# Kernel optimization log

Measured on AMD Instinct MI355X. Metric: run time of the kernel, lower is better.

Reference implementation:

```python
import jax, jax.numpy as jnp
import numpy as np

B, S, DIM = 4, 2048, 512
HEADS, DHEAD = 8, 64
INNER = HEADS * DHEAD


def setup_inputs() -> dict:
    key = jax.random.key(0)
    k1, k2, k3, k4 = jax.random.split(key, 4)
    x = jax.random.normal(k1, (B, S, DIM), dtype=jnp.float32)
    W_qkv = jax.random.normal(k2, (DIM, 3 * INNER), dtype=jnp.float32) * (DIM ** -0.5)
    W_out = jax.random.normal(k3, (INNER, DIM), dtype=jnp.float32) * (INNER ** -0.5)
    b_out = jnp.zeros((DIM,), dtype=jnp.float32)
    # learnable log-temperature, initialized to log(dim_head**-0.5)
    log_temp = jnp.asarray(np.log(DHEAD ** -0.5), dtype=jnp.float32)
    return {"x": x, "W_qkv": W_qkv, "log_temp": log_temp, "W_out": W_out, "b_out": b_out}


def reference(x, W_qkv, log_temp, W_out, b_out):
    b, s, _ = x.shape
    qkv = x @ W_qkv  # [b, s, 3*inner]
    q, k, v = jnp.split(qkv, 3, axis=-1)
    # [b, s, inner] -> [b, h, s, d]
    reshape = lambda t: t.reshape(b, s, HEADS, DHEAD).transpose(0, 2, 1, 3)
    q, k, v = reshape(q), reshape(k), reshape(v)
    dots = jnp.einsum("bhid,bhjd->bhij", q, k) * jnp.exp(log_temp)
    mask_value = -jnp.finfo(dots.dtype).max
    eye = jnp.eye(s, dtype=bool)
    dots = jnp.where(eye, mask_value, dots)
    attn = jax.nn.softmax(dots, axis=-1)
    out = jnp.einsum("bhij,bhjd->bhid", attn, v)
    out = out.transpose(0, 2, 1, 3).reshape(b, s, INNER)
    return out @ W_out + b_out
```

## Files before the change

### kernel.cpp

```cpp
#include <hip/hip_runtime.h>
#include <hip/hip_bf16.h>

#define BB 4
#define SS 2048
#define DIMM 512
#define HH 8
#define DD 64
#define NQKV 1536

typedef float  floatx4 __attribute__((ext_vector_type(4)));
typedef short  bf16x8  __attribute__((ext_vector_type(8)));
typedef short  bf16x4  __attribute__((ext_vector_type(4)));

#define MFMA16(A, B, C) __builtin_amdgcn_mfma_f32_16x16x32_bf16(A, B, C, 0, 0, 0)

__device__ __forceinline__ floatx4 MFMA16K16(bf16x4 a, bf16x4 b, floatx4 c) {
#if __has_builtin(__builtin_amdgcn_mfma_f32_16x16x16bf16_1k)
    return __builtin_amdgcn_mfma_f32_16x16x16bf16_1k(a, b, c, 0, 0, 0);
#else
    floatx4 d;
    asm volatile("v_mfma_f32_16x16x16_bf16 %0, %1, %2, %3"
                 : "=v"(d) : "v"(a), "v"(b), "v"(c));
    return d;
#endif
}

__device__ __forceinline__ unsigned short f2bf(float f) {
    unsigned int u = __float_as_uint(f);
    u += 0x7FFFu + ((u >> 16) & 1u);
    return (unsigned short)(u >> 16);
}

__device__ __forceinline__ unsigned int f2bf_pk(float lo, float hi) {
    float2 f; f.x = lo; f.y = hi;
    __hip_bfloat162 h = __float22bfloat162_rn(f);
    return *reinterpret_cast<unsigned int*>(&h);
}

__device__ __forceinline__ float fast_exp2(float x) {
#if __has_builtin(__builtin_amdgcn_exp2f)
    return __builtin_amdgcn_exp2f(x);
#else
    return __exp2f(x);
#endif
}

__device__ __forceinline__ void gl_lds16(const void* g, void* l) {
    __builtin_amdgcn_global_load_lds(
        (__attribute__((address_space(1))) void*)g,
        (__attribute__((address_space(3))) void*)l,
        16, 0, 0);
}

__global__ __launch_bounds__(256) void k_prep(
    const float* __restrict__ x, const float* __restrict__ W_qkv,
    const float* __restrict__ W_out,
    unsigned short* __restrict__ xb, unsigned short* __restrict__ Wq_t,
    unsigned short* __restrict__ Wo_t) {
    __shared__ float t[32][33];
    int bid = blockIdx.x, tid = threadIdx.x;
    if (bid < 4096) {
        int i = (bid * 256 + tid) * 4;
        float4 v = *(const float4*)(x + i);
        ushort4 o;
        o.x = f2bf(v.x); o.y = f2bf(v.y); o.z = f2bf(v.z); o.w = f2bf(v.w);
        *(ushort4*)(xb + i) = o;
        return;
    }
    const float* in; unsigned short* out; int R = 512, C, bx, by;
    if (bid < 4864) { in = W_qkv; out = Wq_t; C = 1536; int blk = bid - 4096; bx = blk % 48; by = blk / 48; }
    else            { in = W_out; out = Wo_t; C = 512;  int blk = bid - 4864; bx = blk % 16; by = blk / 16; }
    int tx = tid & 31, ty = tid >> 5;
    int c0 = bx * 32, r0 = by * 32;
    for (int i = 0; i < 4; i++) {
        int r = r0 + ty + i * 8;
        t[ty + i * 8][tx] = in[(size_t)r * C + c0 + tx];
    }
    __syncthreads();
    for (int i = 0; i < 4; i++) {
        int cc = c0 + ty + i * 8;
        out[(size_t)cc * R + r0 + tx] = f2bf(t[tx][ty + i * 8]);
    }
}

__global__ __launch_bounds__(256) void k_gemm_qkv(
    const unsigned short* __restrict__ A,
    const unsigned short* __restrict__ Bt,
    const float* __restrict__ log_temp,
    unsigned short* __restrict__ Qb,
    unsigned short* __restrict__ Kb,
    unsigned short* __restrict__ Vt) {
    __shared__ unsigned short smem[2][128 * 64];
    unsigned short* As = smem[0];
    unsigned short* Bs = smem[1];
    const int K = 512;
    int m0 = blockIdx.x * 128, n0 = blockIdx.y * 128;
    int tid = threadIdx.x;
    int w = tid >> 6, lane = tid & 63;
    int c = lane & 15, q4 = lane >> 4;
    int wm = w >> 1, wn = w & 1;
    float qscale = __expf(log_temp[0]) * 1.44269504f;

    floatx4 acc[4][4] = {};

    for (int k0 = 0; k0 < K; k0 += 64) {
        __syncthreads();
        for (int i = 0; i < 4; i++) {
            int cidx = w * 256 + i * 64 + lane;
            int row = cidx >> 3, cc = cidx & 7;
            int gcc = cc ^ (row & 7);
            gl_lds16(A + (size_t)(m0 + row) * K + k0 + gcc * 8,
                     As + (size_t)(w * 256 + i * 64) * 8);
            gl_lds16(Bt + (size_t)(n0 + row) * K + k0 + gcc * 8,
                     Bs + (size_t)(w * 256 + i * 64) * 8);
        }
        __syncthreads();
        bf16x8 aF[2][4], bF[2][4];
        for (int kh = 0; kh < 2; kh++)
            for (int mt = 0; mt < 4; mt++) {
                int row = wm * 64 + mt * 16 + c;
                aF[kh][mt] = *(const bf16x8*)&As[row * 64 + (((kh * 4 + q4) ^ (row & 7)) * 8)];
            }
        for (int kh = 0; kh < 2; kh++)
            for (int nt = 0; nt < 4; nt++) {
                int row = wn * 64 + nt * 16 + c;
                bF[kh][nt] = *(const bf16x8*)&Bs[row * 64 + (((kh * 4 + q4) ^ (row & 7)) * 8)];
            }
        for (int kh = 0; kh < 2; kh++)
            for (int mt = 0; mt < 4; mt++)
                for (int nt = 0; nt < 4; nt++)
                    acc[mt][nt] = MFMA16(aF[kh][mt], bF[kh][nt], acc[mt][nt]);
    }

    if (n0 < 1024) {
        for (int nt = 0; nt < 4; nt++) {
            int n = n0 + wn * 64 + nt * 16 + c;
            int t = n >> 9, inner = n & 511;
            int h = inner >> 6, d = inner & 63;
            for (int mt = 0; mt < 4; mt++) {
                for (int r = 0; r < 4; r++) {
                    int m = m0 + wm * 64 + mt * 16 + q4 * 4 + r;
                    int b = m >> 11, s = m & 2047;
                    int bh = b * 8 + h;
                    float v = acc[mt][nt][r];
                    if (t == 0)  Qb[((size_t)bh * SS + s) * 64 + d] = f2bf(v * qscale);
                    else         Kb[((size_t)bh * SS + s) * 64 + d] = f2bf(v);
                }
            }
        }
    } else {
        unsigned short* T = &smem[0][0];
        int b = m0 >> 11, s_base = m0 & 2047;
        for (int half = 0; half < 2; half++) {
            __syncthreads();
            if (wn == half) {
                for (int nt = 0; nt < 4; nt++)
                    for (int mt = 0; mt < 4; mt++)
                        for (int r = 0; r < 4; r++)
                            T[(nt * 16 + c) * 136 + wm * 64 + mt * 16 + q4 * 4 + r] =
                                f2bf(acc[mt][nt][r]);
            }
            __syncthreads();
            for (int rr = 0; rr < 4; rr++) {
                int nl = w * 16 + rr * 4 + q4;
                int ml = c * 8;
                bf16x8 v = *(const bf16x8*)&T[nl * 136 + ml];
                int n = n0 + half * 64 + nl;
                int h = (n >> 6) - 16, d = n & 63;
                int bh = b * 8 + h;
                *(bf16x8*)(Vt + ((size_t)bh * 64 + d) * SS + s_base + ml) = v;
            }
        }
    }
}

__global__ __launch_bounds__(256, 2) void k_attn(
    const unsigned short* __restrict__ Qb,
    const unsigned short* __restrict__ Kb,
    const unsigned short* __restrict__ Vt,
    unsigned short* __restrict__ AO) {
    __shared__ unsigned short Ks[3][64 * 64];
    __shared__ unsigned short Vs[3][64 * 64];
    int q0 = blockIdx.x * 128;
    int h = blockIdx.y, b = blockIdx.z;
    int bh = b * 8 + h;
    int tid = threadIdx.x, w = tid >> 6, lane = tid & 63;
    int c = lane & 15, q4 = lane >> 4;

    const unsigned short* Kbase = Kb + (size_t)bh * SS * 64;
    const unsigned short* Vbase = Vt + (size_t)bh * 64 * SS;

    bf16x8 qf[2][2];
    for (int mi = 0; mi < 2; mi++) {
        const unsigned short* qp = Qb + ((size_t)bh * SS + q0 + w * 32 + mi * 16 + c) * 64;
        qf[mi][0] = *(const bf16x8*)(qp + q4 * 8);
        qf[mi][1] = *(const bf16x8*)(qp + 32 + q4 * 8);
    }

    const unsigned short* ksrc[2];
    const unsigned short* vsrc[2];
    int ldst[2];
    for (int i = 0; i < 2; i++) {
        int cidx = i * 256 + tid;
        int grow = cidx >> 3, gcc = (cidx & 7) ^ (grow & 7);
        ksrc[i] = Kbase + (size_t)grow * 64 + gcc * 8;
        vsrc[i] = Vbase + (size_t)grow * SS + gcc * 8;
        ldst[i] = (i * 256 + w * 64) * 8;
    }

    for (int i = 0; i < 2; i++) {
        gl_lds16(ksrc[i], &Ks[0][ldst[i]]);
        gl_lds16(vsrc[i], &Vs[0][ldst[i]]);
    }
    for (int i = 0; i < 2; i++) {
        gl_lds16(ksrc[i] + (size_t)64 * 64, &Ks[1][ldst[i]]);
        gl_lds16(vsrc[i] + 64, &Vs[1][ldst[i]]);
    }

    int koff0 = (q4 ^ (c & 7)) * 8;
    int koff1 = ((4 + q4) ^ (c & 7)) * 8;
    int vsub = (q4 & 1) * 4;
    int vchunk0 = (q4 >> 1);

    int mask_j0 = (q0 + w * 32) & ~63;
    int mglob0 = q0 + w * 32 + c;
    int mglob1 = mglob0 + 16;
    floatx4 oacc[2][4] = {};
    float psum0 = 0.f, psum1 = 0.f;

    int buf = 0;
    for (int j0 = 0; j0 < SS; j0 += 64) {
        if (j0 + 64 < SS) {
            asm volatile("s_waitcnt vmcnt(4)" ::: "memory");
        } else {
            asm volatile("s_waitcnt vmcnt(0)" ::: "memory");
        }
        asm volatile("s_barrier" ::: "memory");

        int jn = j0 + 128;
        if (jn < SS) {
            int bufn = buf + 2; if (bufn >= 3) bufn -= 3;
            for (int i = 0; i < 2; i++) {
                gl_lds16(ksrc[i] + (size_t)jn * 64, &Ks[bufn][ldst[i]]);
                gl_lds16(vsrc[i] + jn, &Vs[bufn][ldst[i]]);
            }
        }

        bool diag = (j0 == mask_j0);
        const unsigned short* KsB = Ks[buf];
        const unsigned short* VsB = Vs[buf];

#pragma unroll
        for (int jt = 0; jt < 4; jt++) {
            int rowoff = (jt * 16 + c) * 64;
            bf16x8 kf0 = *(const bf16x8*)&KsB[rowoff + koff0];
            bf16x8 kf1 = *(const bf16x8*)&KsB[rowoff + koff1];
            floatx4 sa0 = {}, sa1 = {};
            sa0 = MFMA16(kf0, qf[0][0], sa0);
            sa0 = MFMA16(kf1, qf[0][1], sa0);
            sa1 = MFMA16(kf0, qf[1][0], sa1);
            sa1 = MFMA16(kf1, qf[1][1], sa1);

            if (diag) {
#pragma unroll
                for (int r = 0; r < 4; r++) {
                    int jg = j0 + jt * 16 + q4 * 4 + r;
                    if (jg == mglob0) sa0[r] = -1e30f;
                    if (jg == mglob1) sa1[r] = -1e30f;
                }
            }

            float e0 = fast_exp2(sa0[0]), e1 = fast_exp2(sa0[1]);
            float e2 = fast_exp2(sa0[2]), e3 = fast_exp2(sa0[3]);
            psum0 += (e0 + e1) + (e2 + e3);
            union { bf16x4 v; unsigned int u[2]; } P0;
            P0.u[0] = f2bf_pk(e0, e1); P0.u[1] = f2bf_pk(e2, e3);
            float f0 = fast_exp2(sa1[0]), f1 = fast_exp2(sa1[1]);
            float f2v = fast_exp2(sa1[2]), f3 = fast_exp2(sa1[3]);
            psum1 += (f0 + f1) + (f2v + f3);
            union { bf16x4 v; unsigned int u[2]; } P1;
            P1.u[0] = f2bf_pk(f0, f1); P1.u[1] = f2bf_pk(f2v, f3);

            int chunk = jt * 2 + vchunk0;
#pragma unroll
            for (int dt = 0; dt < 4; dt++) {
                int vrow = dt * 16 + c;
                bf16x4 vf = *(const bf16x4*)&VsB[vrow * 64 + ((chunk ^ (c & 7)) * 8) + vsub];
                oacc[0][dt] = MFMA16K16(P0.v, vf, oacc[0][dt]);
                oacc[1][dt] = MFMA16K16(P1.v, vf, oacc[1][dt]);
            }
        }
        buf = buf + 1; if (buf >= 3) buf = 0;
    }

    for (int mi = 0; mi < 2; mi++) {
        float l = (mi == 0) ? psum0 : psum1;
        l += __shfl_xor(l, 16);
        l += __shfl_xor(l, 32);
        for (int r = 0; r < 4; r++) {
            float lr = __shfl(l, q4 * 4 + r, 64);
            float inv = 1.0f / lr;
            int s = q0 + w * 32 + mi * 16 + q4 * 4 + r;
            for (int dt = 0; dt < 4; dt++)
                AO[((size_t)b * SS + s) * 512 + h * 64 + dt * 16 + c] =
                    f2bf(oacc[mi][dt][r] * inv);
        }
    }
}

__global__ __launch_bounds__(256) void k_gemm_out(
    const unsigned short* __restrict__ A,
    const unsigned short* __restrict__ Bt,
    const float* __restrict__ bias,
    float* __restrict__ out) {
    __shared__ unsigned short As[64 * 64];
    __shared__ unsigned short Bs[128 * 64];
    const int K = 512;
    int m0 = blockIdx.x * 64, n0 = blockIdx.y * 128;
    int tid = threadIdx.x;
    int w = tid >> 6, lane = tid & 63;
    int c = lane & 15, q4 = lane >> 4;

    floatx4 acc[8] = {};

    for (int k0 = 0; k0 < K; k0 += 64) {
        __syncthreads();
        for (int i = 0; i < 2; i++) {
            int cidx = i * 256 + tid;
            int row = cidx >> 3, cc = cidx & 7;
            int gcc = cc ^ (row & 7);
            gl_lds16(A + (size_t)(m0 + row) * K + k0 + gcc * 8,
                     As + (size_t)(i * 256 + w * 64) * 8);
        }
        for (int i = 0; i < 4; i++) {
            int cidx = i * 256 + tid;
            int row = cidx >> 3, cc = cidx & 7;
            int gcc = cc ^ (row & 7);
            gl_lds16(Bt + (size_t)(n0 + row) * K + k0 + gcc * 8,
                     Bs + (size_t)(i * 256 + w * 64) * 8);
        }
        __syncthreads();
        bf16x8 aF[2], bF[2][8];
        for (int kh = 0; kh < 2; kh++) {
            int row = w * 16 + c;
            aF[kh] = *(const bf16x8*)&As[row * 64 + (((kh * 4 + q4) ^ (row & 7)) * 8)];
        }
        for (int kh = 0; kh < 2; kh++)
            for (int nt = 0; nt < 8; nt++) {
                int row = nt * 16 + c;
                bF[kh][nt] = *(const bf16x8*)&Bs[row * 64 + (((kh * 4 + q4) ^ (row & 7)) * 8)];
            }
        for (int kh = 0; kh < 2; kh++)
            for (int nt = 0; nt < 8; nt++)
                acc[nt] = MFMA16(aF[kh], bF[kh][nt], acc[nt]);
    }

    for (int nt = 0; nt < 8; nt++) {
        int n = n0 + nt * 16 + c;
        float bv = bias[n];
        for (int r = 0; r < 4; r++) {
            int m = m0 + w * 16 + q4 * 4 + r;
            out[(size_t)m * 512 + n] = acc[nt][r] + bv;
        }
    }
}

extern "C" void kernel_launch(void* const* d_in, const int* in_sizes, int n_in,
                              void* d_out, int out_size, void* d_ws, size_t ws_size,
                              hipStream_t stream) {
    const float* x        = (const float*)d_in[0];
    const float* W_qkv    = (const float*)d_in[1];
    const float* log_temp = (const float*)d_in[2];
    const float* W_out    = (const float*)d_in[3];
    const float* b_out    = (const float*)d_in[4];
    float* out = (float*)d_out;

    char* ws = (char*)d_ws;
    unsigned short* xb   = (unsigned short*)(ws + 0);
    unsigned short* Wq_t = (unsigned short*)(ws + 8388608);
    unsigned short* Wo_t = (unsigned short*)(ws + 9961472);
    unsigned short* Qb   = (unsigned short*)(ws + 10485760);
    unsigned short* Kb   = (unsigned short*)(ws + 18874368);
    unsigned short* Vt   = (unsigned short*)(ws + 27262976);
    unsigned short* AO   = (unsigned short*)(ws + 35651584);

    k_prep<<<5120, 256, 0, stream>>>(x, W_qkv, W_out, xb, Wq_t, Wo_t);
    k_gemm_qkv<<<dim3(64, 12), 256, 0, stream>>>(xb, Wq_t, log_temp, Qb, Kb, Vt);
    k_attn<<<dim3(16, 8, 4), 256, 0, stream>>>(Qb, Kb, Vt, AO);
    k_gemm_out<<<dim3(128, 4), 256, 0, stream>>>(AO, Wo_t, b_out, out);
}
```

Measured before the change: 168.5 us.

## Stage Q/K epilogue through LDS and compute softmax row sums with MFMA

Result: no change. 170.1 us (+1.0%).

```diff
diff --git a/kernel.cpp b/kernel.cpp
--- a/kernel.cpp
+++ b/kernel.cpp
@@ -132,25 +132,34 @@
                     acc[mt][nt] = MFMA16(aF[kh][mt], bF[kh][nt], acc[mt][nt]);
     }
 
+    int b = m0 >> 11, s_base = m0 & 2047;
     if (n0 < 1024) {
-        for (int nt = 0; nt < 4; nt++) {
-            int n = n0 + wn * 64 + nt * 16 + c;
-            int t = n >> 9, inner = n & 511;
-            int h = inner >> 6, d = inner & 63;
-            for (int mt = 0; mt < 4; mt++) {
-                for (int r = 0; r < 4; r++) {
-                    int m = m0 + wm * 64 + mt * 16 + q4 * 4 + r;
-                    int b = m >> 11, s = m & 2047;
-                    int bh = b * 8 + h;
-                    float v = acc[mt][nt][r];
-                    if (t == 0)  Qb[((size_t)bh * SS + s) * 64 + d] = f2bf(v * qscale);
-                    else         Kb[((size_t)bh * SS + s) * 64 + d] = f2bf(v);
-                }
+        bool isQ = (n0 < 512);
+        float scale = isQ ? qscale : 1.0f;
+        unsigned short* dst = isQ ? Qb : Kb;
+        unsigned short* T = &smem[0][0];
+        for (int half = 0; half < 2; half++) {
+            __syncthreads();
+            if (wn == half) {
+                for (int nt = 0; nt < 4; nt++)
+                    for (int mt = 0; mt < 4; mt++)
+                        for (int r = 0; r < 4; r++)
+                            T[(wm * 64 + mt * 16 + q4 * 4 + r) * 72 + nt * 16 + c] =
+                                f2bf(acc[mt][nt][r] * scale);
+            }
+            __syncthreads();
+            int n_base = n0 + half * 64;
+            int hq = (n_base >> 6) & 7;
+            int bh = b * 8 + hq;
+            int gg = tid & 7;
+            for (int rr = 0; rr < 4; rr++) {
+                int m = (tid >> 3) + 32 * rr;
+                bf16x8 v = *(const bf16x8*)&T[m * 72 + gg * 8];
+                *(bf16x8*)(dst + ((size_t)bh * SS + s_base + m) * 64 + gg * 8) = v;
             }
         }
     } else {
         unsigned short* T = &smem[0][0];
-        int b = m0 >> 11, s_base = m0 & 2047;
         for (int half = 0; half < 2; half++) {
             __syncthreads();
             if (wn == half) {
@@ -196,6 +205,11 @@
         qf[mi][0] = *(const bf16x8*)(qp + q4 * 8);
         qf[mi][1] = *(const bf16x8*)(qp + 32 + q4 * 8);
     }
+    bf16x4 ones4;
+    {
+        short o1 = (c == 0) ? (short)0x3F80 : (short)0;
+        for (int j = 0; j < 4; j++) ones4[j] = o1;
+    }
 
     const unsigned short* ksrc[2];
     const unsigned short* vsrc[2];
@@ -226,7 +240,7 @@
     int mglob0 = q0 + w * 32 + c;
     int mglob1 = mglob0 + 16;
     floatx4 oacc[2][4] = {};
-    float psum0 = 0.f, psum1 = 0.f;
+    floatx4 lacc[2] = {};
 
     int buf = 0;
     for (int j0 = 0; j0 < SS; j0 += 64) {
@@ -270,16 +284,14 @@
                 }
             }
 
-            float e0 = fast_exp2(sa0[0]), e1 = fast_exp2(sa0[1]);
-            float e2 = fast_exp2(sa0[2]), e3 = fast_exp2(sa0[3]);
-            psum0 += (e0 + e1) + (e2 + e3);
-            union { bf16x4 v; unsigned int u[2]; } P0;
-            P0.u[0] = f2bf_pk(e0, e1); P0.u[1] = f2bf_pk(e2, e3);
-            float f0 = fast_exp2(sa1[0]), f1 = fast_exp2(sa1[1]);
-            float f2v = fast_exp2(sa1[2]), f3 = fast_exp2(sa1[3]);
-            psum1 += (f0 + f1) + (f2v + f3);
-            union { bf16x4 v; unsigned int u[2]; } P1;
-            P1.u[0] = f2bf_pk(f0, f1); P1.u[1] = f2bf_pk(f2v, f3);
+            union { bf16x4 v; unsigned int u[2]; } P0, P1;
+            P0.u[0] = f2bf_pk(fast_exp2(sa0[0]), fast_exp2(sa0[1]));
+            P0.u[1] = f2bf_pk(fast_exp2(sa0[2]), fast_exp2(sa0[3]));
+            P1.u[0] = f2bf_pk(fast_exp2(sa1[0]), fast_exp2(sa1[1]));
+            P1.u[1] = f2bf_pk(fast_exp2(sa1[2]), fast_exp2(sa1[3]));
+
+            lacc[0] = MFMA16K16(P0.v, ones4, lacc[0]);
+            lacc[1] = MFMA16K16(P1.v, ones4, lacc[1]);
 
             int chunk = jt * 2 + vchunk0;
 #pragma unroll
@@ -294,11 +306,8 @@
     }
 
     for (int mi = 0; mi < 2; mi++) {
-        float l = (mi == 0) ? psum0 : psum1;
-        l += __shfl_xor(l, 16);
-        l += __shfl_xor(l, 32);
         for (int r = 0; r < 4; r++) {
-            float lr = __shfl(l, q4 * 4 + r, 64);
+            float lr = __shfl(lacc[mi][r], q4 << 4, 64);
             float inv = 1.0f / lr;
             int s = q0 + w * 32 + mi * 16 + q4 * 4 + r;
             for (int dt = 0; dt < 4; dt++)
```
